# Performance work log

Hardware: AMD Instinct MI355X
Metric: run time of the kernel (lower is better)

## Reference

```python
import jax, jax.numpy as jnp
import numpy as np

N_SKU, N_WH, N_SUP = 100000, 5000, 2000
D_IN, D_OUT, H = 128, 64, 4
DH = D_OUT // H  # 16
E_INTRA, E_CROSS = 400000, 200000
EPS_LN = 1e-5


def setup_inputs() -> dict:
    key = jax.random.key(0)
    ks = jax.random.split(key, 40)
    f32 = jnp.float32

    def edges(k, E, n_src, n_dst):
        k1, k2 = jax.random.split(k)
        return jnp.stack([
            jax.random.randint(k1, (E,), 0, n_src),
            jax.random.randint(k2, (E,), 0, n_dst),
        ]).astype(jnp.int32)

    inp = {
        'x_sku': jax.random.normal(ks[0], (N_SKU, D_IN), f32),
        'x_wh': jax.random.normal(ks[1], (N_WH, D_IN), f32),
        'x_sup': jax.random.normal(ks[2], (N_SUP, D_IN), f32),
    }
    names = ['plant', 'pg', 'sg', 'st', 'ship', 'supply']
    for i, nm in enumerate(names):
        inp['W_' + nm] = jax.random.normal(ks[3 + 2 * i], (D_IN, D_OUT), f32) * 0.05
        inp['a_' + nm] = jax.random.normal(ks[4 + 2 * i], (2 * DH,), f32) * 0.05
    inp['proj_W'] = jax.random.normal(ks[20], (2 * D_OUT, D_OUT), f32) * 0.05
    inp['proj_b'] = jnp.zeros((D_OUT,), f32)
    inp['ln_g'] = jnp.ones((D_OUT,), f32)
    inp['ln_b'] = jnp.zeros((D_OUT,), f32)
    inp['res_W'] = jax.random.normal(ks[21], (D_IN, D_OUT), f32) * 0.05
    inp['ei_plant'] = edges(ks[22], E_INTRA, N_SKU, N_SKU)
    inp['ei_pg'] = edges(ks[23], E_INTRA, N_SKU, N_SKU)
    inp['ei_sg'] = edges(ks[24], E_INTRA, N_SKU, N_SKU)
    inp['ei_st'] = edges(ks[25], E_INTRA, N_SKU, N_SKU)
    inp['ei_ship'] = edges(ks[26], E_CROSS, N_SKU, N_WH)
    inp['ei_supply'] = edges(ks[27], E_CROSS, N_SKU, N_SUP)
    return inp


def _gat_conv(src_feat, dst_feat, ei, W, a, num_dst):
    """One-edge-type multi-head GAT: ELU edge scores, per-dst softmax, scatter-add."""
    src_i, dst_i = ei[0], ei[1]
    h_src = (src_feat @ W).reshape(-1, H, DH)  # [N_src, H, dh]
    h_dst = (dst_feat @ W).reshape(-1, H, DH)  # [N_dst, H, dh]
    hs = h_src[src_i]  # [E, H, dh] gather
    hd = h_dst[dst_i]  # [E, H, dh]
    # a^T [h_src || h_dst], shared attention vector across heads
    e = jax.nn.elu(hs @ a[:DH] + hd @ a[DH:])  # [E, H]
    # numerically stable scatter-softmax over edges grouped by dst node
    e_max = jax.lax.stop_gradient(jax.ops.segment_max(e, dst_i, num_segments=num_dst))
    e_max = jnp.where(jnp.isfinite(e_max), e_max, 0.0)
    exp_e = jnp.exp(e - e_max[dst_i])
    denom = jax.ops.segment_sum(exp_e, dst_i, num_segments=num_dst)
    alpha = exp_e / (denom[dst_i] + 1e-12)  # [E, H]
    out = jax.ops.segment_sum(alpha[..., None] * hs, dst_i, num_segments=num_dst)
    return out.reshape(num_dst, D_OUT)


def reference(x_sku, x_wh, x_sup,
              W_plant, a_plant, W_pg, a_pg, W_sg, a_sg, W_st, a_st,
              W_ship, a_ship, W_supply, a_supply,
              proj_W, proj_b, ln_g, ln_b, res_W,
              ei_plant, ei_pg, ei_sg, ei_st, ei_ship, ei_supply):
    # branch A (intra sku->sku edge types), summed into sku accumulator
    oa_sku = (_gat_conv(x_sku, x_sku, ei_plant, W_plant, a_plant, N_SKU)
              + _gat_conv(x_sku, x_sku, ei_pg, W_pg, a_pg, N_SKU)
              + _gat_conv(x_sku, x_sku, ei_sg, W_sg, a_sg, N_SKU)
              + _gat_conv(x_sku, x_sku, ei_st, W_st, a_st, N_SKU))
    ob_sku = jnp.zeros((N_SKU, D_OUT), x_sku.dtype)
    # branch B (cross edge types)
    oa_wh = jnp.zeros((N_WH, D_OUT), x_wh.dtype)
    ob_wh = _gat_conv(x_sku, x_wh, ei_ship, W_ship, a_ship, N_WH)
    oa_sup = jnp.zeros((N_SUP, D_OUT), x_sup.dtype)
    ob_sup = _gat_conv(x_sku, x_sup, ei_supply, W_supply, a_supply, N_SUP)

    def finish(x, oa, ob):
        y = jnp.concatenate([oa, ob], axis=-1) @ proj_W + proj_b + x @ res_W
        mu = y.mean(-1, keepdims=True)
        var = ((y - mu) ** 2).mean(-1, keepdims=True)
        return (y - mu) / jnp.sqrt(var + EPS_LN) * ln_g + ln_b

    return (finish(x_sku, oa_sku, ob_sku),
            finish(x_wh, oa_wh, ob_wh),
            finish(x_sup, oa_sup, ob_sup))
```

## Files before the change

kernel.cpp:

```cpp
#include <hip/hip_runtime.h>
#include <hip/hip_bf16.h>
#include <cstdint>

#define NS 100000
#define NW 5000
#define NPS 2000
#define DI 128
#define DO 64
#define NSTRIPS (NS/16)
#define NFLAT (4*NS + NW + NPS)
#define NWPAD 5008
#define NBUK 134
#define BCAP 20480
#define CHUNK 8192

#define B_CONV 6688
#define B_PACK 304
#define B_SWH  157
#define B_SSUP 63

typedef unsigned short bfu;
typedef __attribute__((ext_vector_type(8))) short s8v;
typedef __attribute__((ext_vector_type(4))) float f4v;

__device__ inline bfu f2bf(float f) {
  uint32_t u = __float_as_uint(f);
  u = (u + 0x7FFFu + ((u >> 16) & 1u)) >> 16;
  return (bfu)u;
}
__device__ inline float bf2f(bfu u) {
  return __uint_as_float((uint32_t)u << 16);
}

struct ESeg { const int* ei[6]; int E[6]; int Ecum[7]; };

__device__ inline void buk_of(int t, int d, int& b, int& loc) {
  if (t < 4)       { int f = d * 4 + t; b = f >> 12;        loc = f & 4095; }
  else if (t == 4) { b = 98 + (d >> 8);                     loc = d & 255; }
  else             { b = 118 + (d >> 7);                    loc = d & 127; }
}

struct PackA {
  const float* W[6]; const float* a[6];
  const float* resW; const float* projW;
  bfu* Bp; bfu* Rp; bfu* Pp;
};

struct K1Args {
  ESeg S; int* gCur; uint32_t* binned; int ETOT; int nbin;
  const float* x0; bfu* o0; int n0;
  const float* x1; bfu* o1; int n1;
  const float* x2; bfu* o2; int n2;
  PackA P;
  const float* xwh; const float* xsup; float* sd_wh; float* sd_sup;
};

__device__ void bin_body(const K1Args& A, int bid) {
  __shared__ int cnt[NBUK];
  __shared__ int runb[NBUK];
  const ESeg& S = A.S;
  int tid = threadIdx.x;
  int gbase = bid * CHUNK;
  if (tid < NBUK) cnt[tid] = 0;
  __syncthreads();
  #pragma unroll 4
  for (int i = 0; i < CHUNK / 256; ++i) {
    int g = gbase + i * 256 + tid;
    if (g < A.ETOT) {
      int t = 0;
      #pragma unroll
      for (int k = 0; k < 5; ++k) t += (g >= S.Ecum[k + 1]);
      int e = g - S.Ecum[t];
      int d = S.ei[t][S.E[t] + e];
      int b, loc; buk_of(t, d, b, loc);
      atomicAdd(&cnt[b], 1);
    }
  }
  __syncthreads();
  if (tid < NBUK) { runb[tid] = atomicAdd(&A.gCur[tid], cnt[tid]); cnt[tid] = 0; }
  __syncthreads();
  #pragma unroll 4
  for (int i = 0; i < CHUNK / 256; ++i) {
    int g = gbase + i * 256 + tid;
    if (g < A.ETOT) {
      int t = 0;
      #pragma unroll
      for (int k = 0; k < 5; ++k) t += (g >= S.Ecum[k + 1]);
      int e = g - S.Ecum[t];
      int sv = S.ei[t][e];
      int d  = S.ei[t][S.E[t] + e];
      int b, loc; buk_of(t, d, b, loc);
      int pos = runb[b] + atomicAdd(&cnt[b], 1);
      if (pos < BCAP)
        A.binned[(size_t)b * BCAP + pos] = ((uint32_t)loc << 17) | (uint32_t)sv;
    }
  }
}

__device__ void convert_body(const K1Args& A, int bid) {
  int t = bid * 256 + threadIdx.x;
  const float* x; bfu* o; int i;
  if (t < A.n0) { x = A.x0; o = A.o0; i = t; }
  else if (t < A.n0 + A.n1) { x = A.x1; o = A.o1; i = t - A.n0; }
  else if (t < A.n0 + A.n1 + A.n2) { x = A.x2; o = A.o2; i = t - A.n0 - A.n1; }
  else return;
  const float4* p = (const float4*)x + (size_t)i * 2;
  float4 a = p[0], b = p[1];
  uint4 v;
  v.x = (uint32_t)f2bf(a.x) | ((uint32_t)f2bf(a.y) << 16);
  v.y = (uint32_t)f2bf(a.z) | ((uint32_t)f2bf(a.w) << 16);
  v.z = (uint32_t)f2bf(b.x) | ((uint32_t)f2bf(b.y) << 16);
  v.w = (uint32_t)f2bf(b.z) | ((uint32_t)f2bf(b.w) << 16);
  ((uint4*)o)[i] = v;
}

__device__ void pack_body(const PackA& P, int bid) {
  int t = bid * 256 + threadIdx.x;
  if (t < 61440) {
    int ty = t / 10240, rem = t % 10240;
    int r = rem / 128, k = rem % 128;
    const float* W = P.W[ty]; const float* a = P.a[ty];
    float v = 0.f;
    if (r < 64) v = W[k * 64 + r];
    else if (r < 72) {
      int h = (r - 64) & 3;
      const float* av = (r < 68) ? a : (a + 16);
      #pragma unroll
      for (int m = 0; m < 16; ++m) v += W[k * 64 + h * 16 + m] * av[m];
    }
    P.Bp[ty * 10240 + rem] = f2bf(v);
  } else if (t < 69632) {
    int i = t - 61440; int j = i / 128, k = i % 128;
    P.Rp[i] = f2bf(P.resW[k * 64 + j]);
  } else if (t < 77824) {
    int i = t - 69632; int j = i / 128, k = i % 128;
    P.Pp[i] = f2bf(P.projW[k * 64 + j]);
  }
}

__device__ void scores_body(const float* __restrict__ x, const float* __restrict__ W,
                            const float* __restrict__ a, float* __restrict__ sdst,
                            int N, int bid, int nblk) {
  int tid = threadIdx.x;
  int lane = tid & 63;
  float wa[4] = {0.f, 0.f, 0.f, 0.f}, wb[4] = {0.f, 0.f, 0.f, 0.f};
  for (int m = 0; m < 16; ++m) {
    float av = a[16 + m];
    #pragma unroll
    for (int h = 0; h < 4; ++h) {
      wa[h] += W[lane * 64 + h * 16 + m] * av;
      wb[h] += W[(64 + lane) * 64 + h * 16 + m] * av;
    }
  }
  int w  = (bid * 256 + tid) >> 6;
  int nw = (nblk * 256) >> 6;
  for (int n = w; n < N; n += nw) {
    float xa = x[(size_t)n * 128 + lane], xc = x[(size_t)n * 128 + 64 + lane];
    float4 r;
    r.x = xa * wa[0] + xc * wb[0]; r.y = xa * wa[1] + xc * wb[1];
    r.z = xa * wa[2] + xc * wb[2]; r.w = xa * wa[3] + xc * wb[3];
    #pragma unroll
    for (int m = 1; m < 64; m <<= 1) {
      r.x += __shfl_xor(r.x, m); r.y += __shfl_xor(r.y, m);
      r.z += __shfl_xor(r.z, m); r.w += __shfl_xor(r.w, m);
    }
    if (lane == 0) ((float4*)sdst)[n] = r;
  }
}

__global__ __launch_bounds__(256) void k_front(K1Args A) {
  int bid = blockIdx.x;
  if (bid < A.nbin) { bin_body(A, bid); return; }
  bid -= A.nbin;
  if (bid < B_CONV) { convert_body(A, bid); return; }
  bid -= B_CONV;
  if (bid < B_PACK) { pack_body(A.P, bid); return; }
  bid -= B_PACK;
  if (bid < B_SWH) { scores_body(A.xwh, A.P.W[4], A.P.a[4], A.sd_wh, NW, bid, B_SWH); return; }
  bid -= B_SWH;
  scores_body(A.xsup, A.P.W[5], A.P.a[5], A.sd_sup, NPS, bid, B_SSUP);
}

__global__ __launch_bounds__(1024) void k_csr(const int* __restrict__ gCur,
    const uint32_t* __restrict__ binned, int* __restrict__ offs,
    int* __restrict__ ssorted) {
  __shared__ int hist[4096];
  __shared__ int wsc[16];
  __shared__ int bbase_s, cnt_s;
  int b = blockIdx.x, tid = threadIdx.x;
  int lane = tid & 63, wid = tid >> 6;
  if (tid == 0) {
    int bb = 0, own = 0;
    for (int k = 0; k < NBUK; ++k) {
      int c = min(gCur[k], BCAP);
      if (k < b) bb += c;
      if (k == b) own = c;
    }
    bbase_s = bb; cnt_s = own;
  }
  #pragma unroll
  for (int k = 0; k < 4; ++k) hist[tid * 4 + k] = 0;
  __syncthreads();
  int cnt = cnt_s, bbase = bbase_s;
  const uint32_t* bk = binned + (size_t)b * BCAP;
  for (int i = tid; i < cnt; i += 1024)
    atomicAdd(&hist[bk[i] >> 17], 1);
  __syncthreads();
  int t4 = tid * 4;
  int v0 = hist[t4], v1 = hist[t4 + 1], v2 = hist[t4 + 2], v3 = hist[t4 + 3];
  int tsum = v0 + v1 + v2 + v3;
  int inc = tsum;
  #pragma unroll
  for (int d = 1; d < 64; d <<= 1) { int tt = __shfl_up(inc, d); if (lane >= d) inc += tt; }
  if (lane == 63) wsc[wid] = inc;
  __syncthreads();
  int wpre = 0;
  for (int k = 0; k < wid; ++k) wpre += wsc[k];
  int excl = inc - tsum + wpre;
  hist[t4] = excl;
  hist[t4 + 1] = excl + v0;
  hist[t4 + 2] = excl + v0 + v1;
  hist[t4 + 3] = excl + v0 + v1 + v2;
  __syncthreads();
  int sbase, nslots;
  if (b < 98)        { sbase = b << 12;                nslots = min(4096, 4 * NS - sbase); }
  else if (b < 118)  { int lb = (b - 98) << 8;  sbase = 4 * NS + lb;      nslots = min(256, NW - lb); }
  else               { int lb = (b - 118) << 7; sbase = 4 * NS + NW + lb; nslots = min(128, NPS - lb); }
  for (int i = tid; i < nslots; i += 1024) offs[sbase + i] = bbase + hist[i];
  if (b == NBUK - 1 && tid == 0) offs[NFLAT] = bbase + cnt;
  __syncthreads();
  for (int i = tid; i < cnt; i += 1024) {
    uint32_t v = bk[i];
    int p = atomicAdd(&hist[v >> 17], 1);
    ssorted[bbase + p] = (int)(v & 0x1FFFFu);
  }
}

struct GemmArgs {
  const bfu* xb; const bfu* Bp;
  bfu* hbAll; float* ssAll; float* sdAll; int nstrips;
};
__global__ __launch_bounds__(256, 2) void k_gemm(GemmArgs G) {
  int p = blockIdx.x >> 9;
  int bloc = blockIdx.x & 511;
  const bfu* Bp0 = G.Bp + (size_t)(2 * p) * 10240;
  const bfu* Bp1 = G.Bp + (size_t)(2 * p + 1) * 10240;
  bfu* hb0 = G.hbAll + (size_t)(2 * p) * NS * 64;
  bfu* hb1 = G.hbAll + (size_t)(2 * p + 1) * NS * 64;
  float* ss0 = G.ssAll + (size_t)(2 * p) * NS * 4;
  float* ss1 = G.ssAll + (size_t)(2 * p + 1) * NS * 4;
  float* sd0 = G.sdAll + (size_t)(2 * p) * NS * 4;
  float* sd1 = G.sdAll + (size_t)(2 * p + 1) * NS * 4;
  int lane = threadIdx.x & 63;
  int l15 = lane & 15, q = lane >> 4;
  int w  = (int)((bloc * 256 + threadIdx.x) >> 6);
  int nw = (512 * 256) >> 6;
  s8v bfr[10][4];
  #pragma unroll
  for (int nt = 0; nt < 5; ++nt)
    #pragma unroll
    for (int kq = 0; kq < 4; ++kq) {
      bfr[nt][kq]     = *(const s8v*)(Bp0 + (size_t)(nt * 16 + l15) * 128 + kq * 32 + q * 8);
      bfr[5 + nt][kq] = *(const s8v*)(Bp1 + (size_t)(nt * 16 + l15) * 128 + kq * 32 + q * 8);
    }
  for (int s = w; s < G.nstrips; s += nw) {
    int mb = s * 16;
    f4v acc[10];
    #pragma unroll
    for (int u = 0; u < 10; ++u) acc[u] = (f4v){0.f, 0.f, 0.f, 0.f};
    const bfu* ar = G.xb + (size_t)(mb + l15) * 128 + q * 8;
    #pragma unroll
    for (int kq = 0; kq < 4; ++kq) {
      s8v af = *(const s8v*)(ar + kq * 32);
      #pragma unroll
      for (int u = 0; u < 10; ++u)
        acc[u] = __builtin_amdgcn_mfma_f32_16x16x32_bf16(af, bfr[u][kq], acc[u], 0, 0, 0);
    }
    #pragma unroll
    for (int u = 0; u < 10; ++u) {
      int nt = (u < 5) ? u : u - 5;
      bfu* hb = (u < 5) ? hb0 : hb1;
      float* ssrc = (u < 5) ? ss0 : ss1;
      float* sdst = (u < 5) ? sd0 : sd1;
      int c = nt * 16 + l15;
      #pragma unroll
      for (int r = 0; r < 4; ++r) {
        int node = mb + q * 4 + r;
        float v = acc[u][r];
        if (c < 64)      hb[(size_t)node * 64 + c] = f2bf(v);
        else if (c < 68) ssrc[(size_t)node * 4 + (c - 64)] = v;
        else if (c < 72) sdst[(size_t)node * 4 + (c - 68)] = v;
      }
    }
  }
}

struct AggArgs {
  const int* offs; const int* srcs;
  const bfu* hbAll;
  const float* ssAll;
  const float* sdAll;
  const float* sd_wh; const float* sd_sup;
  bfu* osku; bfu* owh; bfu* osup;
};

__global__ __launch_bounds__(256) void k_megaagg(AggArgs A) {
  int lane = threadIdx.x & 63;
  int q = lane >> 4, m = lane & 15, h = m >> 2;
  int qsh = q << 4;
  int w  = (int)((blockIdx.x * 256 + threadIdx.x) >> 6);
  int nw = (int)((gridDim.x * 256) >> 6);
  for (int n = w; n < NS + NW + NPS; n += nw) {
    if (n < NS) {
      const int* ob = A.offs + (size_t)n * 4;
      int4 o = *(const int4*)ob;
      int o4 = ob[4];
      int sb = (q == 0) ? o.x : (q == 1) ? o.y : (q == 2) ? o.z : o.w;
      int se = (q == 0) ? o.y : (q == 1) ? o.z : (q == 2) ? o.w : o4;
      int len = se - sb;
      int maxlen = max(max(o.y - o.x, o.z - o.y), max(o.w - o.z, o4 - o.w));
      float sdv = A.sdAll[((size_t)q * NS + n) * 4 + h];
      uint32_t tbase = (uint32_t)q * (uint32_t)NS;
      float den = 0.f, a0 = 0.f, a1 = 0.f, a2 = 0.f, a3 = 0.f;
      for (int j0 = 0; j0 < maxlen; j0 += 16) {
        int ei = j0 + m;
        int sidx = (ei < len) ? A.srcs[sb + ei] : 0;
        int gmax = min(16, maxlen - j0);
        for (int jj = 0; jj < gmax; jj += 8) {
          float sc[8]; uint2 hv[8]; int vj[8];
          #pragma unroll
          for (int i = 0; i < 8; ++i) {
            int j = jj + i;
            int s = __shfl(sidx, qsh + j);
            vj[i] = (j0 + j) < len;
            uint32_t nb = tbase + (uint32_t)s;
            sc[i] = A.ssAll[nb * 4u + (uint32_t)h];
            hv[i] = *(const uint2*)(A.hbAll + nb * 64u + (uint32_t)(m * 4));
          }
          #pragma unroll
          for (int i = 0; i < 8; ++i) {
            float e = sc[i] + sdv;
            e = e > 0.f ? e : (__expf(e) - 1.f);
            float wgt = vj[i] ? __expf(e) : 0.f;
            den += wgt;
            a0 = fmaf(__uint_as_float(hv[i].x << 16), wgt, a0);
            a1 = fmaf(__uint_as_float(hv[i].x & 0xffff0000u), wgt, a1);
            a2 = fmaf(__uint_as_float(hv[i].y << 16), wgt, a2);
            a3 = fmaf(__uint_as_float(hv[i].y & 0xffff0000u), wgt, a3);
          }
        }
      }
      float inv = __builtin_amdgcn_rcpf(den + 1e-12f);
      float r0 = a0 * inv, r1 = a1 * inv, r2 = a2 * inv, r3 = a3 * inv;
      r0 += __shfl_xor(r0, 16); r0 += __shfl_xor(r0, 32);
      r1 += __shfl_xor(r1, 16); r1 += __shfl_xor(r1, 32);
      r2 += __shfl_xor(r2, 16); r2 += __shfl_xor(r2, 32);
      r3 += __shfl_xor(r3, 16); r3 += __shfl_xor(r3, 32);
      if (q == 0) {
        uint2 pk;
        pk.x = (uint32_t)f2bf(r0) | ((uint32_t)f2bf(r1) << 16);
        pk.y = (uint32_t)f2bf(r2) | ((uint32_t)f2bf(r3) << 16);
        *(uint2*)(A.osku + (size_t)n * 64 + m * 4) = pk;
      }
    } else {
      int tt, nl; const float* sd; bfu* op;
      int fi;
      if (n < NS + NW) { tt = 4; nl = n - NS; fi = 4 * NS + nl; sd = A.sd_wh; op = A.owh + (size_t)nl * 64; }
      else { tt = 5; nl = n - NS - NW; fi = 4 * NS + NW + nl; sd = A.sd_sup; op = A.osup + (size_t)nl * 64; }
      int beg = A.offs[fi], end = A.offs[fi + 1];
      uint32_t tbase = (uint32_t)tt * (uint32_t)NS;
      float sdv = sd[(size_t)nl * 4 + h];
      float den = 0.f, a0 = 0.f, a1 = 0.f, a2 = 0.f, a3 = 0.f;
      for (int cb = beg; cb < end; cb += 64) {
        int rem = min(64, end - cb);
        int sidx = (lane < rem) ? A.srcs[cb + lane] : 0;
        for (int jb = 0; jb < rem; jb += 32) {
          float sc[8]; uint2 hv[8]; int vj[8];
          #pragma unroll
          for (int i = 0; i < 8; ++i) {
            int eidx = jb + 4 * i + q;
            int s = __shfl(sidx, eidx);
            vj[i] = eidx < rem;
            uint32_t nb = tbase + (uint32_t)s;
            sc[i] = A.ssAll[nb * 4u + (uint32_t)h];
            hv[i] = *(const uint2*)(A.hbAll + nb * 64u + (uint32_t)(m * 4));
          }
          #pragma unroll
          for (int i = 0; i < 8; ++i) {
            float e = sc[i] + sdv;
            e = e > 0.f ? e : (__expf(e) - 1.f);
            float wgt = vj[i] ? __expf(e) : 0.f;
            den += wgt;
            a0 = fmaf(__uint_as_float(hv[i].x << 16), wgt, a0);
            a1 = fmaf(__uint_as_float(hv[i].x & 0xffff0000u), wgt, a1);
            a2 = fmaf(__uint_as_float(hv[i].y << 16), wgt, a2);
            a3 = fmaf(__uint_as_float(hv[i].y & 0xffff0000u), wgt, a3);
          }
        }
      }
      den += __shfl_xor(den, 16); den += __shfl_xor(den, 32);
      a0 += __shfl_xor(a0, 16); a0 += __shfl_xor(a0, 32);
      a1 += __shfl_xor(a1, 16); a1 += __shfl_xor(a1, 32);
      a2 += __shfl_xor(a2, 16); a2 += __shfl_xor(a2, 32);
      a3 += __shfl_xor(a3, 16); a3 += __shfl_xor(a3, 32);
      float inv = __builtin_amdgcn_rcpf(den + 1e-12f);
      if (q == 0) {
        uint2 pk;
        pk.x = (uint32_t)f2bf(a0 * inv) | ((uint32_t)f2bf(a1 * inv) << 16);
        pk.y = (uint32_t)f2bf(a2 * inv) | ((uint32_t)f2bf(a3 * inv) << 16);
        *(uint2*)(op + m * 4) = pk;
      }
    }
  }
}

struct FinArgs {
  const bfu* agg0; const bfu* agg1; const bfu* agg2;
  const bfu* x0; const bfu* x1; const bfu* x2;
  float* out0; float* out1; float* out2;
  const bfu* Pp; const bfu* Rp;
  const float* pb; const float* g; const float* bb;
  int bcut0, bcut1;
};

__global__ __launch_bounds__(256) void k_finish(FinArgs F) {
  int bid = blockIdx.x;
  int role = (bid >= F.bcut0) + (bid >= F.bcut1);
  int b0 = (role == 0) ? 0 : (role == 1) ? F.bcut0 : F.bcut1;
  int nb = (role == 0) ? F.bcut0 : (role == 1) ? (F.bcut1 - F.bcut0) : ((int)gridDim.x - F.bcut1);
  int bloc = bid - b0;
  const bfu* aggb = (role == 0) ? F.agg0 : (role == 1) ? F.agg1 : F.agg2;
  const bfu* xbf  = (role == 0) ? F.x0 : (role == 1) ? F.x1 : F.x2;
  float* outp     = (role == 0) ? F.out0 : (role == 1) ? F.out1 : F.out2;
  int koff    = (role == 0) ? 0 : 64;
  int N       = (role == 0) ? NS : (role == 1) ? NW : NPS;
  int nstrips = (role == 0) ? NSTRIPS : (role == 1) ? (NWPAD / 16) : (NPS / 16);

  int lane = threadIdx.x & 63, l15 = lane & 15, q = lane >> 4;
  int w  = (int)((bloc * 256 + threadIdx.x) >> 6);
  int nw = nb << 2;
  s8v bP[4][2], bR[4][4];
  float pbv[4], gv[4], bv[4];
  #pragma unroll
  for (int c = 0; c < 4; ++c) {
    const bfu* pr = F.Pp + (size_t)(c * 16 + l15) * 128 + koff;
    bP[c][0] = *(const s8v*)(pr + q * 8);
    bP[c][1] = *(const s8v*)(pr + 32 + q * 8);
    const bfu* rr = F.Rp + (size_t)(c * 16 + l15) * 128;
    #pragma unroll
    for (int kq = 0; kq < 4; ++kq) bR[c][kq] = *(const s8v*)(rr + kq * 32 + q * 8);
    pbv[c] = F.pb[c * 16 + l15]; gv[c] = F.g[c * 16 + l15]; bv[c] = F.bb[c * 16 + l15];
  }
  for (int s = w; s < nstrips; s += nw) {
    int mb = s * 16;
    const bfu* ar = aggb + (size_t)(mb + l15) * 64 + q * 8;
    const bfu* xr = xbf + (size_t)(mb + l15) * 128 + q * 8;
    s8v a0 = *(const s8v*)ar, a1 = *(const s8v*)(ar + 32);
    s8v x0 = *(const s8v*)xr, x1 = *(const s8v*)(xr + 32),
        x2 = *(const s8v*)(xr + 64), x3 = *(const s8v*)(xr + 96);
    f4v acc[4];
    #pragma unroll
    for (int c = 0; c < 4; ++c) {
      acc[c] = (f4v){0.f, 0.f, 0.f, 0.f};
      acc[c] = __builtin_amdgcn_mfma_f32_16x16x32_bf16(a0, bP[c][0], acc[c], 0, 0, 0);
      acc[c] = __builtin_amdgcn_mfma_f32_16x16x32_bf16(a1, bP[c][1], acc[c], 0, 0, 0);
      acc[c] = __builtin_amdgcn_mfma_f32_16x16x32_bf16(x0, bR[c][0], acc[c], 0, 0, 0);
      acc[c] = __builtin_amdgcn_mfma_f32_16x16x32_bf16(x1, bR[c][1], acc[c], 0, 0, 0);
      acc[c] = __builtin_amdgcn_mfma_f32_16x16x32_bf16(x2, bR[c][2], acc[c], 0, 0, 0);
      acc[c] = __builtin_amdgcn_mfma_f32_16x16x32_bf16(x3, bR[c][3], acc[c], 0, 0, 0);
    }
    #pragma unroll
    for (int r = 0; r < 4; ++r) {
      int row = mb + q * 4 + r;
      float y0 = acc[0][r] + pbv[0], y1 = acc[1][r] + pbv[1];
      float y2 = acc[2][r] + pbv[2], y3 = acc[3][r] + pbv[3];
      float s1 = y0 + y1 + y2 + y3;
      s1 += __shfl_xor(s1, 1); s1 += __shfl_xor(s1, 2);
      s1 += __shfl_xor(s1, 4); s1 += __shfl_xor(s1, 8);
      float mu = s1 * 0.015625f;
      float d0 = y0 - mu, d1 = y1 - mu, d2 = y2 - mu, d3 = y3 - mu;
      float s2 = d0 * d0 + d1 * d1 + d2 * d2 + d3 * d3;
      s2 += __shfl_xor(s2, 1); s2 += __shfl_xor(s2, 2);
      s2 += __shfl_xor(s2, 4); s2 += __shfl_xor(s2, 8);
      float rs = rsqrtf(s2 * 0.015625f + 1e-5f);
      if (row < N) {
        float* orow = outp + (size_t)row * 64 + l15;
        orow[0]  = d0 * rs * gv[0] + bv[0];
        orow[16] = d1 * rs * gv[1] + bv[1];
        orow[32] = d2 * rs * gv[2] + bv[2];
        orow[48] = d3 * rs * gv[3] + bv[3];
      }
    }
  }
}

extern "C" void kernel_launch(void* const* d_in, const int* in_sizes, int n_in,
                              void* d_out, int out_size, void* d_ws, size_t ws_size,
                              hipStream_t stream) {
  const float* x_sku = (const float*)d_in[0];
  const float* x_wh  = (const float*)d_in[1];
  const float* x_sup = (const float*)d_in[2];
  const float* Wt[6]; const float* at[6];
  for (int t = 0; t < 6; ++t) { Wt[t] = (const float*)d_in[3 + 2 * t]; at[t] = (const float*)d_in[4 + 2 * t]; }
  const float* projW = (const float*)d_in[15];
  const float* projb = (const float*)d_in[16];
  const float* lng   = (const float*)d_in[17];
  const float* lnb   = (const float*)d_in[18];
  const float* resW  = (const float*)d_in[19];
  const int* ei[6]; int Et[6];
  for (int t = 0; t < 6; ++t) { ei[t] = (const int*)d_in[20 + t]; Et[t] = in_sizes[20 + t] / 2; }
  float* out = (float*)d_out;

  int ETOT = 0;
  for (int t = 0; t < 6; ++t) ETOT += Et[t];

  char* ws = (char*)d_ws;
  size_t off = 0;
  auto alloc = [&](size_t bytes) { off = (off + 255) & ~(size_t)255; void* p = ws + off; off += bytes; return p; };

  bfu*  xb      = (bfu*)alloc((size_t)NS * DI * 2);
  bfu*  xb_wh   = (bfu*)alloc((size_t)NWPAD * DI * 2);
  bfu*  xb_sup  = (bfu*)alloc((size_t)NPS * DI * 2);
  bfu*  Bp      = (bfu*)alloc((size_t)6 * 80 * 128 * 2);
  bfu*  Rp      = (bfu*)alloc((size_t)64 * 128 * 2);
  bfu*  Pp      = (bfu*)alloc((size_t)64 * 128 * 2);
  bfu*  hbAll   = (bfu*)alloc((size_t)6 * NS * 64 * 2);
  float* ssAll  = (float*)alloc((size_t)6 * NS * 4 * 4);
  float* sdAll  = (float*)alloc((size_t)6 * NS * 4 * 4);
  float* sdst_wh  = (float*)alloc((size_t)NW * 4 * 4);
  float* sdst_sup = (float*)alloc((size_t)NPS * 4 * 4);
  size_t agg_bytes = ((size_t)NS + NWPAD + NPS) * 64 * 2;
  size_t bin_bytes = (size_t)NBUK * BCAP * 4;
  char* un = (char*)alloc(agg_bytes > bin_bytes ? agg_bytes : bin_bytes);
  bfu* agg_sku = (bfu*)un;
  bfu* agg_wh  = agg_sku + (size_t)NS * 64;
  bfu* agg_sup = agg_wh + (size_t)NWPAD * 64;
  uint32_t* binned = (uint32_t*)un;
  int* gCur    = (int*)alloc(256 * 4);
  int* offsb   = (int*)alloc((size_t)(NFLAT + 1) * 4);
  int* ssorted = (int*)alloc((size_t)ETOT * 4);

  hipMemsetAsync(gCur, 0, NBUK * 4, stream);

  K1Args K;
  K.S.Ecum[0] = 0;
  for (int t = 0; t < 6; ++t) { K.S.ei[t] = ei[t]; K.S.E[t] = Et[t]; K.S.Ecum[t + 1] = K.S.Ecum[t] + Et[t]; }
  K.gCur = gCur; K.binned = binned; K.ETOT = ETOT;
  K.nbin = (ETOT + CHUNK - 1) / CHUNK;
  K.x0 = x_sku; K.o0 = xb;     K.n0 = NS * 16;
  K.x1 = x_wh;  K.o1 = xb_wh;  K.n1 = NW * 16;
  K.x2 = x_sup; K.o2 = xb_sup; K.n2 = NPS * 16;
  for (int t = 0; t < 6; ++t) { K.P.W[t] = Wt[t]; K.P.a[t] = at[t]; }
  K.P.resW = resW; K.P.projW = projW; K.P.Bp = Bp; K.P.Rp = Rp; K.P.Pp = Pp;
  K.xwh = x_wh; K.xsup = x_sup; K.sd_wh = sdst_wh; K.sd_sup = sdst_sup;
  int gfront = K.nbin + B_CONV + B_PACK + B_SWH + B_SSUP;
  k_front<<<gfront, 256, 0, stream>>>(K);

  k_csr<<<NBUK, 1024, 0, stream>>>(gCur, binned, offsb, ssorted);

  GemmArgs G;
  G.xb = xb; G.Bp = Bp; G.hbAll = hbAll; G.ssAll = ssAll; G.sdAll = sdAll; G.nstrips = NSTRIPS;
  k_gemm<<<1536, 256, 0, stream>>>(G);

  AggArgs A;
  A.offs = offsb; A.srcs = ssorted;
  A.hbAll = hbAll; A.ssAll = ssAll; A.sdAll = sdAll;
  A.sd_wh = sdst_wh; A.sd_sup = sdst_sup;
  A.osku = agg_sku; A.owh = agg_wh; A.osup = agg_sup;
  k_megaagg<<<(NS + NW + NPS + 3) / 4, 256, 0, stream>>>(A);

  FinArgs F;
  F.agg0 = agg_sku; F.agg1 = agg_wh; F.agg2 = agg_sup;
  F.x0 = xb; F.x1 = xb_wh; F.x2 = xb_sup;
  F.out0 = out; F.out1 = out + (size_t)NS * 64; F.out2 = out + (size_t)(NS + NW) * 64;
  F.Pp = Pp; F.Rp = Rp; F.pb = projb; F.g = lng; F.bb = lnb;
  F.bcut0 = 1563; F.bcut1 = 1563 + 79;
  k_finish<<<1563 + 79 + 32, 256, 0, stream>>>(F);
}
```

Before: 378.8 us.

## Fuse CSR build and GEMM into one launch; dedupe per-edge attention score math

Merges the CSR-sort kernel (reworked for 256 threads, 16 bins per thread, with a parallel prefix over bucket counts) and the projection GEMM into a single k_mid launch, so the two independent stages can run concurrently and one kernel launch is removed. In the aggregation kernel, each edge's attention score load, ELU and exp were previously computed redundantly by all 16 lanes of a quarter-wave. They are now computed once per (edge, head) and broadcast with shuffles. This cuts transcendental and score-load work at the cost of extra shuffles and a lower-occupancy CSR block.

```diff
diff --git a/kernel.cpp b/kernel.cpp
--- a/kernel.cpp
+++ b/kernel.cpp
@@ -181,68 +181,68 @@
   scores_body(A.xsup, A.P.W[5], A.P.a[5], A.sd_sup, NPS, bid, B_SSUP);
 }
 
-__global__ __launch_bounds__(1024) void k_csr(const int* __restrict__ gCur,
-    const uint32_t* __restrict__ binned, int* __restrict__ offs,
-    int* __restrict__ ssorted) {
+struct MidArgs {
+  const int* gCur; const uint32_t* binned; int* offs; int* ssorted;
+  const bfu* xb; const bfu* Bp;
+  bfu* hbAll; float* ssAll; float* sdAll; int nstrips;
+};
+
+__device__ void csr_body(const MidArgs& M, int b) {
   __shared__ int hist[4096];
-  __shared__ int wsc[16];
+  __shared__ int wq[4];
+  __shared__ int wsc[4];
   __shared__ int bbase_s, cnt_s;
-  int b = blockIdx.x, tid = threadIdx.x;
+  int tid = threadIdx.x;
   int lane = tid & 63, wid = tid >> 6;
-  if (tid == 0) {
-    int bb = 0, own = 0;
-    for (int k = 0; k < NBUK; ++k) {
-      int c = min(gCur[k], BCAP);
-      if (k < b) bb += c;
-      if (k == b) own = c;
-    }
-    bbase_s = bb; cnt_s = own;
-  }
-  #pragma unroll
-  for (int k = 0; k < 4; ++k) hist[tid * 4 + k] = 0;
+  int cthis = (tid < NBUK) ? min(M.gCur[tid], BCAP) : 0;
+  int incx = cthis;
+  #pragma unroll
+  for (int d = 1; d < 64; d <<= 1) { int t = __shfl_up(incx, d); if (lane >= d) incx += t; }
+  if (lane == 63) wq[wid] = incx;
+  #pragma unroll
+  for (int k = 0; k < 16; ++k) hist[tid * 16 + k] = 0;
+  __syncthreads();
+  int wp = 0;
+  for (int k = 0; k < wid; ++k) wp += wq[k];
+  if (tid == b) { int inclusive = incx + wp; bbase_s = inclusive - cthis; cnt_s = cthis; }
   __syncthreads();
   int cnt = cnt_s, bbase = bbase_s;
-  const uint32_t* bk = binned + (size_t)b * BCAP;
-  for (int i = tid; i < cnt; i += 1024)
+  const uint32_t* bk = M.binned + (size_t)b * BCAP;
+  for (int i = tid; i < cnt; i += 256)
     atomicAdd(&hist[bk[i] >> 17], 1);
   __syncthreads();
-  int t4 = tid * 4;
-  int v0 = hist[t4], v1 = hist[t4 + 1], v2 = hist[t4 + 2], v3 = hist[t4 + 3];
-  int tsum = v0 + v1 + v2 + v3;
+  int t16 = tid * 16;
+  int v[16], tsum = 0;
+  #pragma unroll
+  for (int k = 0; k < 16; ++k) { v[k] = hist[t16 + k]; tsum += v[k]; }
   int inc = tsum;
   #pragma unroll
-  for (int d = 1; d < 64; d <<= 1) { int tt = __shfl_up(inc, d); if (lane >= d) inc += tt; }
+  for (int d = 1; d < 64; d <<= 1) { int t = __shfl_up(inc, d); if (lane >= d) inc += t; }
   if (lane == 63) wsc[wid] = inc;
   __syncthreads();
   int wpre = 0;
   for (int k = 0; k < wid; ++k) wpre += wsc[k];
-  int excl = inc - tsum + wpre;
-  hist[t4] = excl;
-  hist[t4 + 1] = excl + v0;
-  hist[t4 + 2] = excl + v0 + v1;
-  hist[t4 + 3] = excl + v0 + v1 + v2;
+  int run = inc - tsum + wpre;
+  #pragma unroll
+  for (int k = 0; k < 16; ++k) { hist[t16 + k] = run; run += v[k]; }
   __syncthreads();
   int sbase, nslots;
   if (b < 98)        { sbase = b << 12;                nslots = min(4096, 4 * NS - sbase); }
   else if (b < 118)  { int lb = (b - 98) << 8;  sbase = 4 * NS + lb;      nslots = min(256, NW - lb); }
   else               { int lb = (b - 118) << 7; sbase = 4 * NS + NW + lb; nslots = min(128, NPS - lb); }
-  for (int i = tid; i < nslots; i += 1024) offs[sbase + i] = bbase + hist[i];
-  if (b == NBUK - 1 && tid == 0) offs[NFLAT] = bbase + cnt;
-  __syncthreads();
-  for (int i = tid; i < cnt; i += 1024) {
-    uint32_t v = bk[i];
-    int p = atomicAdd(&hist[v >> 17], 1);
-    ssorted[bbase + p] = (int)(v & 0x1FFFFu);
-  }
-}
-
-struct GemmArgs {
-  const bfu* xb; const bfu* Bp;
-  bfu* hbAll; float* ssAll; float* sdAll; int nstrips;
-};
-__global__ __launch_bounds__(256, 2) void k_gemm(GemmArgs G) {
-  int p = blockIdx.x >> 9;
-  int bloc = blockIdx.x & 511;
+  for (int i = tid; i < nslots; i += 256) M.offs[sbase + i] = bbase + hist[i];
+  if (b == NBUK - 1 && tid == 0) M.offs[NFLAT] = bbase + cnt;
+  __syncthreads();
+  for (int i = tid; i < cnt; i += 256) {
+    uint32_t vv = bk[i];
+    int p = atomicAdd(&hist[vv >> 17], 1);
+    M.ssorted[bbase + p] = (int)(vv & 0x1FFFFu);
+  }
+}
+
+__device__ void gemm_body(const MidArgs& G, int bloc) {
+  int p = bloc >> 9;
+  int bsub = bloc & 511;
   const bfu* Bp0 = G.Bp + (size_t)(2 * p) * 10240;
   const bfu* Bp1 = G.Bp + (size_t)(2 * p + 1) * 10240;
   bfu* hb0 = G.hbAll + (size_t)(2 * p) * NS * 64;
@@ -253,7 +253,7 @@
   float* sd1 = G.sdAll + (size_t)(2 * p + 1) * NS * 4;
   int lane = threadIdx.x & 63;
   int l15 = lane & 15, q = lane >> 4;
-  int w  = (int)((bloc * 256 + threadIdx.x) >> 6);
+  int w  = (int)((bsub * 256 + threadIdx.x) >> 6);
   int nw = (512 * 256) >> 6;
   s8v bfr[10][4];
   #pragma unroll
@@ -295,6 +295,12 @@
   }
 }
 
+__global__ __launch_bounds__(256, 2) void k_mid(MidArgs M) {
+  int bid = blockIdx.x;
+  if (bid < NBUK) { csr_body(M, bid); return; }
+  gemm_body(M, bid - NBUK);
+}
+
 struct AggArgs {
   const int* offs; const int* srcs;
   const bfu* hbAll;
@@ -307,7 +313,10 @@
 __global__ __launch_bounds__(256) void k_megaagg(AggArgs A) {
   int lane = threadIdx.x & 63;
   int q = lane >> 4, m = lane & 15, h = m >> 2;
+  int hh = m & 3;
+  int i0 = m >> 2;
   int qsh = q << 4;
+  int sl0 = qsh + h;
   int w  = (int)((blockIdx.x * 256 + threadIdx.x) >> 6);
   int nw = (int)((gridDim.x * 256) >> 6);
   for (int n = w; n < NS + NW + NPS; n += nw) {
@@ -319,7 +328,7 @@
       int se = (q == 0) ? o.y : (q == 1) ? o.z : (q == 2) ? o.w : o4;
       int len = se - sb;
       int maxlen = max(max(o.y - o.x, o.z - o.y), max(o.w - o.z, o4 - o.w));
-      float sdv = A.sdAll[((size_t)q * NS + n) * 4 + h];
+      float sdq = A.sdAll[((size_t)q * NS + n) * 4 + hh];
       uint32_t tbase = (uint32_t)q * (uint32_t)NS;
       float den = 0.f, a0 = 0.f, a1 = 0.f, a2 = 0.f, a3 = 0.f;
       for (int j0 = 0; j0 < maxlen; j0 += 16) {
@@ -327,21 +336,26 @@
         int sidx = (ei < len) ? A.srcs[sb + ei] : 0;
         int gmax = min(16, maxlen - j0);
         for (int jj = 0; jj < gmax; jj += 8) {
-          float sc[8]; uint2 hv[8]; int vj[8];
+          int sA = __shfl(sidx, qsh + jj + i0);
+          int sB = __shfl(sidx, qsh + jj + 4 + i0);
+          float scA = A.ssAll[(tbase + (uint32_t)sA) * 4u + (uint32_t)hh];
+          float scB = A.ssAll[(tbase + (uint32_t)sB) * 4u + (uint32_t)hh];
+          float eA = scA + sdq, eB = scB + sdq;
+          eA = eA > 0.f ? eA : (__expf(eA) - 1.f);
+          eB = eB > 0.f ? eB : (__expf(eB) - 1.f);
+          float wA = (j0 + jj + i0)     < len ? __expf(eA) : 0.f;
+          float wB = (j0 + jj + 4 + i0) < len ? __expf(eB) : 0.f;
+          uint2 hv[8]; float wg[8];
           #pragma unroll
           for (int i = 0; i < 8; ++i) {
-            int j = jj + i;
-            int s = __shfl(sidx, qsh + j);
-            vj[i] = (j0 + j) < len;
+            int s = __shfl(sidx, qsh + jj + i);
             uint32_t nb = tbase + (uint32_t)s;
-            sc[i] = A.ssAll[nb * 4u + (uint32_t)h];
             hv[i] = *(const uint2*)(A.hbAll + nb * 64u + (uint32_t)(m * 4));
+            wg[i] = __shfl((i & 4) ? wB : wA, sl0 + ((i & 3) << 2));
           }
           #pragma unroll
           for (int i = 0; i < 8; ++i) {
-            float e = sc[i] + sdv;
-            e = e > 0.f ? e : (__expf(e) - 1.f);
-            float wgt = vj[i] ? __expf(e) : 0.f;
+            float wgt = wg[i];
             den += wgt;
             a0 = fmaf(__uint_as_float(hv[i].x << 16), wgt, a0);
             a1 = fmaf(__uint_as_float(hv[i].x & 0xffff0000u), wgt, a1);
@@ -369,27 +383,33 @@
       else { tt = 5; nl = n - NS - NW; fi = 4 * NS + NW + nl; sd = A.sd_sup; op = A.osup + (size_t)nl * 64; }
       int beg = A.offs[fi], end = A.offs[fi + 1];
       uint32_t tbase = (uint32_t)tt * (uint32_t)NS;
-      float sdv = sd[(size_t)nl * 4 + h];
+      float sdq = sd[(size_t)nl * 4 + hh];
       float den = 0.f, a0 = 0.f, a1 = 0.f, a2 = 0.f, a3 = 0.f;
       for (int cb = beg; cb < end; cb += 64) {
         int rem = min(64, end - cb);
         int sidx = (lane < rem) ? A.srcs[cb + lane] : 0;
         for (int jb = 0; jb < rem; jb += 32) {
-          float sc[8]; uint2 hv[8]; int vj[8];
+          int eA = jb + 4 * i0 + q;
+          int sA = __shfl(sidx, eA);
+          int sB = __shfl(sidx, eA + 16);
+          float scA = A.ssAll[(tbase + (uint32_t)sA) * 4u + (uint32_t)hh];
+          float scB = A.ssAll[(tbase + (uint32_t)sB) * 4u + (uint32_t)hh];
+          float fA = scA + sdq, fB = scB + sdq;
+          fA = fA > 0.f ? fA : (__expf(fA) - 1.f);
+          fB = fB > 0.f ? fB : (__expf(fB) - 1.f);
+          float wA = (eA)      < rem ? __expf(fA) : 0.f;
+          float wB = (eA + 16) < rem ? __expf(fB) : 0.f;
+          uint2 hv[8]; float wg[8];
           #pragma unroll
           for (int i = 0; i < 8; ++i) {
-            int eidx = jb + 4 * i + q;
-            int s = __shfl(sidx, eidx);
-            vj[i] = eidx < rem;
+            int s = __shfl(sidx, jb + 4 * i + q);
             uint32_t nb = tbase + (uint32_t)s;
-            sc[i] = A.ssAll[nb * 4u + (uint32_t)h];
             hv[i] = *(const uint2*)(A.hbAll + nb * 64u + (uint32_t)(m * 4));
+            wg[i] = __shfl((i & 4) ? wB : wA, sl0 + ((i & 3) << 2));
           }
           #pragma unroll
           for (int i = 0; i < 8; ++i) {
-            float e = sc[i] + sdv;
-            e = e > 0.f ? e : (__expf(e) - 1.f);
-            float wgt = vj[i] ? __expf(e) : 0.f;
+            float wgt = wg[i];
             den += wgt;
             a0 = fmaf(__uint_as_float(hv[i].x << 16), wgt, a0);
             a1 = fmaf(__uint_as_float(hv[i].x & 0xffff0000u), wgt, a1);
@@ -556,11 +576,10 @@
   int gfront = K.nbin + B_CONV + B_PACK + B_SWH + B_SSUP;
   k_front<<<gfront, 256, 0, stream>>>(K);
 
-  k_csr<<<NBUK, 1024, 0, stream>>>(gCur, binned, offsb, ssorted);
-
-  GemmArgs G;
-  G.xb = xb; G.Bp = Bp; G.hbAll = hbAll; G.ssAll = ssAll; G.sdAll = sdAll; G.nstrips = NSTRIPS;
-  k_gemm<<<1536, 256, 0, stream>>>(G);
+  MidArgs M;
+  M.gCur = gCur; M.binned = binned; M.offs = offsb; M.ssorted = ssorted;
+  M.xb = xb; M.Bp = Bp; M.hbAll = hbAll; M.ssAll = ssAll; M.sdAll = sdAll; M.nstrips = NSTRIPS;
+  k_mid<<<NBUK + 1536, 256, 0, stream>>>(M);
 
   AggArgs A;
   A.offs = offsb; A.srcs = ssorted;
```

Result: no change. 382.3 us (+0.9%).
